# Kernel tuning notes

Hardware: AMD Instinct MI355X
Metric: run time of the kernel (lower is better)

## Reference

```python
import jax, jax.numpy as jnp
import numpy as np

NUM_HEADS = 12
EPS = 1e-6


def setup_inputs() -> dict:
    key = jax.random.key(0)
    k1, k2, k3, k4, k5 = jax.random.split(key, 5)
    B, N, C = 8, 4096, 768
    scale = 1.0 / np.sqrt(C)
    return {
        "x": jax.random.normal(k1, (B, N, C), dtype=jnp.float32),
        "W_qkv": jax.random.normal(k2, (C, 3 * C), dtype=jnp.float32) * scale,
        "b_qkv": jax.random.normal(k3, (3 * C,), dtype=jnp.float32) * 0.02,
        "W_proj": jax.random.normal(k4, (C, C), dtype=jnp.float32) * scale,
        "b_proj": jax.random.normal(k5, (C,), dtype=jnp.float32) * 0.02,
    }


def reference(x, W_qkv, b_qkv, W_proj, b_proj):
    B, N, C = x.shape
    H = NUM_HEADS
    D = C // H
    # qkv projection -> (3, B, H, N, D)
    qkv = (x @ W_qkv + b_qkv).reshape(B, N, 3, H, D).transpose(2, 0, 3, 1, 4)
    q, k, v = qkv[0], qkv[1], qkv[2]
    q = jax.nn.sigmoid(q)
    k = jax.nn.sigmoid(k)
    ksum = k.sum(axis=2)  # [B,H,D]
    qsum = q.sum(axis=2)  # [B,H,D]
    # incoming/outgoing flow normalizers, [B,H,N]
    sink_incoming = 1.0 / (jnp.einsum('bhnd,bhd->bhn', q + EPS, ksum + EPS) + EPS)
    source_outgoing = 1.0 / (jnp.einsum('bhnd,bhd->bhn', k + EPS, qsum + EPS) + EPS)
    conserved_sink = jnp.einsum(
        'bhnd,bhd->bhn', q + EPS, (k * source_outgoing[..., None]).sum(axis=2) + EPS) + EPS
    conserved_source = jnp.einsum(
        'bhnd,bhd->bhn', k + EPS, (q * sink_incoming[..., None]).sum(axis=2) + EPS) + EPS
    conserved_source = jnp.clip(conserved_source, -1.0, 1.0)
    sink_allocation = jax.nn.sigmoid(conserved_sink * (float(N) / float(N)))
    source_competition = jax.nn.softmax(conserved_source, axis=-1) * float(N)
    # linear attention: kv = k^T @ (v * competition), [B,H,D,D]
    kv = jnp.einsum('bhnd,bhne->bhde', k, v * source_competition[..., None])
    x_update = jnp.einsum('bhnd,bhde->bhne', q, kv)
    x_update = x_update * sink_incoming[..., None] * sink_allocation[..., None]
    out = x_update.transpose(0, 2, 1, 3).reshape(B, N, C)
    out = out @ W_proj + b_proj
    return jax.nn.sigmoid(2.0 * out)
```

## Files before the change

### kernel.cpp

```cpp
#include <hip/hip_runtime.h>
#include <stdint.h>

#define EPSF 1e-6f

typedef unsigned short u16;
typedef __attribute__((ext_vector_type(8))) short short8;
typedef __attribute__((ext_vector_type(4))) float f32x4;

__device__ __forceinline__ float us2f(u16 u) {
  union { float f; unsigned int i; } c; c.i = ((unsigned int)u) << 16; return c.f;
}
__device__ __forceinline__ u16 f2bfu(float f) {
  union { float f; unsigned int i; } c; c.f = f;
  unsigned int i = c.i;
  return (u16)((i + 0x7FFFu + ((i >> 16) & 1u)) >> 16);
}
__device__ __forceinline__ float sigm(float x) { return 1.f / (1.f + __expf(-x)); }

typedef __attribute__((address_space(3))) unsigned int lds_u32;
typedef const __attribute__((address_space(1))) unsigned int glb_u32;
__device__ __forceinline__ void gl_lds16(const u16* g, u16* l) {
  __builtin_amdgcn_global_load_lds((glb_u32*)g, (lds_u32*)l, 16, 0, 0);
}

__global__ void k_cvt_x(const float* __restrict__ in, u16* __restrict__ out) {
  const int i = blockIdx.x * 256 + threadIdx.x;
  float4 v = ((const float4*)in)[i];
  ushort4 o;
  o.x = f2bfu(v.x); o.y = f2bfu(v.y); o.z = f2bfu(v.z); o.w = f2bfu(v.w);
  ((ushort4*)out)[i] = o;
}

__global__ void k_transpose(const float* __restrict__ in, u16* __restrict__ out, int R, int C) {
  __shared__ float tile[32][33];
  const int tx = threadIdx.x & 31, ty = threadIdx.x >> 5;
  const int c0 = blockIdx.x << 5, r0 = blockIdx.y << 5;
  for (int i = ty; i < 32; i += 8) tile[i][tx] = in[(size_t)(r0 + i) * C + c0 + tx];
  __syncthreads();
  for (int i = ty; i < 32; i += 8) out[(size_t)(c0 + i) * R + r0 + tx] = f2bfu(tile[tx][i]);
}

template <int MODE>
__global__ __launch_bounds__(512, 2) void k_gemm(
    const u16* __restrict__ A, const u16* __restrict__ BT,
    const float* __restrict__ bias,
    u16* __restrict__ qkvo, float* __restrict__ qsum, float* __restrict__ ksum,
    float* __restrict__ outf)
{
  __shared__ __align__(16) u16 smem[65536];
  const int tid = threadIdx.x;
  const int lane = tid & 63;
  const int wid = tid >> 6;
  const int wm = wid >> 2, wn = wid & 3;
  const int nx = gridDim.x;
  int lid = blockIdx.y * nx + blockIdx.x;
  const int q8 = (nx * gridDim.y) >> 3;
  lid = (lid & 7) * q8 + (lid >> 3);
  const int m0 = (lid / nx) << 8;
  const int n0 = (lid % nx) << 8;

  const int rowS = tid >> 2;
  const int sub  = tid & 3;
  const int subx = sub ^ ((rowS >> 1) & 3);
  const u16* gA = A  + (size_t)(m0 + rowS) * 768 + (subx << 3);
  const u16* gB = BT + (size_t)(n0 + rowS) * 768 + (subx << 3);
  const int dstc = tid << 3;

  const int r16 = lane & 15;
  const int sgrp = lane >> 4;
  int offA[8], offB[4];
#pragma unroll
  for (int mi = 0; mi < 8; ++mi) {
    const int ra = (wm << 7) + (mi << 4) + r16;
    offA[mi] = ra * 32 + ((sgrp ^ ((ra >> 1) & 3)) << 3);
  }
#pragma unroll
  for (int nj = 0; nj < 4; ++nj) {
    const int rb = (wn << 6) + (nj << 4) + r16;
    offB[nj] = rb * 32 + ((sgrp ^ ((rb >> 1) & 3)) << 3);
  }

  f32x4 acc[8][4];
#pragma unroll
  for (int i = 0; i < 8; ++i)
#pragma unroll
    for (int j = 0; j < 4; ++j) acc[i][j] = (f32x4){0.f, 0.f, 0.f, 0.f};

#define STAGE(kh)                                                   \
  do {                                                              \
    const int khs = ((kh) > 23 ? 23 : (kh)) << 5;                   \
    const int so = ((kh) & 3) << 13;                                \
    gl_lds16(gA + khs,         &smem[so + dstc]);                   \
    gl_lds16(gA + 98304 + khs, &smem[so + dstc + 4096]);            \
    gl_lds16(gB + khs,         &smem[32768 + so + dstc]);           \
    gl_lds16(gB + 98304 + khs, &smem[32768 + so + dstc + 4096]);    \
  } while (0)

  STAGE(0); STAGE(1); STAGE(2);

  for (int kh = 0; kh < 24; ++kh) {
    asm volatile("s_waitcnt vmcnt(8)" ::: "memory");
    __builtin_amdgcn_s_barrier();
    __builtin_amdgcn_sched_barrier(0);
    STAGE(kh + 3);
    const u16* pa = &smem[(kh & 3) << 13];
    const u16* pb = pa + 32768;
    short8 bf[4];
#pragma unroll
    for (int nj = 0; nj < 4; ++nj) bf[nj] = *(const short8*)(pb + offB[nj]);
    __builtin_amdgcn_s_setprio(1);
#pragma unroll
    for (int mi = 0; mi < 8; ++mi) {
      const short8 av = *(const short8*)(pa + offA[mi]);
#pragma unroll
      for (int nj = 0; nj < 4; ++nj)
        acc[mi][nj] = __builtin_amdgcn_mfma_f32_16x16x32_bf16(av, bf[nj], acc[mi][nj], 0, 0, 0);
    }
    __builtin_amdgcn_s_setprio(0);
  }
#undef STAGE
  asm volatile("s_waitcnt vmcnt(0)" ::: "memory");

  if (MODE == 0) {
    const int colc = n0 + (wn << 6);
    const bool sg = (colc < 1536);
    float jsum[4] = {0.f, 0.f, 0.f, 0.f};
#pragma unroll
    for (int mi = 0; mi < 8; ++mi) {
      const int rowb = m0 + (wm << 7) + (mi << 4) + ((lane >> 4) << 2);
#pragma unroll
      for (int nj = 0; nj < 4; ++nj) {
        const int col = colc + (nj << 4) + r16;
        const float bcol = bias[col];
        if (sg) {
#pragma unroll
          for (int rg = 0; rg < 4; ++rg) {
            const float val = sigm(acc[mi][nj][rg] + bcol);
            jsum[nj] += val;
            qkvo[(size_t)(rowb + rg) * 2304 + col] = f2bfu(val);
          }
        } else {
#pragma unroll
          for (int rg = 0; rg < 4; ++rg)
            qkvo[(size_t)(rowb + rg) * 2304 + col] = f2bfu(acc[mi][nj][rg] + bcol);
        }
      }
    }
    if (sg) {
#pragma unroll
      for (int nj = 0; nj < 4; ++nj) {
        jsum[nj] += __shfl_xor(jsum[nj], 16, 64);
        jsum[nj] += __shfl_xor(jsum[nj], 32, 64);
      }
      if (lane < 16) {
        const int b12 = (m0 >> 12) * 12;
        float* sdst = (colc >= 768) ? ksum : qsum;
        const int cb = (colc >= 768) ? colc - 768 : colc;
#pragma unroll
        for (int nj = 0; nj < 4; ++nj)
          atomicAdd(&sdst[(b12 << 6) + cb + (nj << 4) + r16], jsum[nj]);
      }
    }
  } else {
#pragma unroll
    for (int mi = 0; mi < 8; ++mi) {
      const int rowb = m0 + (wm << 7) + (mi << 4) + ((lane >> 4) << 2);
#pragma unroll
      for (int nj = 0; nj < 4; ++nj) {
        const int col = n0 + (wn << 6) + (nj << 4) + r16;
        const float bcol = bias[col];
#pragma unroll
        for (int rg = 0; rg < 4; ++rg)
          outf[(size_t)(rowb + rg) * 768 + col] = sigm(2.f * (acc[mi][nj][rg] + bcol));
      }
    }
  }
}

__global__ __launch_bounds__(256) void k_flow1(
    const u16* __restrict__ qkv,
    const float* __restrict__ qsum, const float* __restrict__ ksum,
    float* __restrict__ si_out, float* __restrict__ qsi, float* __restrict__ kso)
{
  const int bh = blockIdx.x >> 3, sp = blockIdx.x & 7;
  const int tid = threadIdx.x;
  const int grp = tid >> 3;
  const int d0 = (tid & 7) << 3;
  const u16* base = qkv + (size_t)(bh / 12) * 4096 * 2304 + (bh % 12) * 64;

  float ke[8], qe[8];
#pragma unroll
  for (int u = 0; u < 8; ++u) {
    ke[u] = ksum[(bh << 6) + d0 + u] + EPSF;
    qe[u] = qsum[(bh << 6) + d0 + u] + EPSF;
  }
  float Sk = 0.f, Sq = 0.f;
#pragma unroll
  for (int u = 0; u < 8; ++u) { Sk += ke[u]; Sq += qe[u]; }
#pragma unroll
  for (int m = 1; m < 8; m <<= 1) { Sk += __shfl_xor(Sk, m, 64); Sq += __shfl_xor(Sq, m, 64); }
  const float cK = EPSF * Sk + EPSF;
  const float cQ = EPSF * Sq + EPSF;

  float aq[8], ak[8];
#pragma unroll
  for (int u = 0; u < 8; ++u) { aq[u] = 0.f; ak[u] = 0.f; }

  const int nbase = sp << 9;
  for (int it = 0; it < 16; ++it) {
    const int n = nbase + (it << 5) + grp;
    const u16* rp = base + (size_t)n * 2304 + d0;
    short8 q8 = *(const short8*)(rp);
    short8 k8 = *(const short8*)(rp + 768);
    float dq = 0.f, dk = 0.f;
#pragma unroll
    for (int u = 0; u < 8; ++u) {
      dq += us2f((u16)q8[u]) * ke[u];
      dk += us2f((u16)k8[u]) * qe[u];
    }
#pragma unroll
    for (int m = 1; m < 8; m <<= 1) { dq += __shfl_xor(dq, m, 64); dk += __shfl_xor(dk, m, 64); }
    const float si = 1.f / (dq + cK);
    const float so = 1.f / (dk + cQ);
    if ((tid & 7) == 0) si_out[(bh << 12) + n] = si;
#pragma unroll
    for (int u = 0; u < 8; ++u) {
      aq[u] += us2f((u16)q8[u]) * si;
      ak[u] += us2f((u16)k8[u]) * so;
    }
  }
  __shared__ float redq[32][68];
  __shared__ float redk[32][68];
#pragma unroll
  for (int u = 0; u < 8; ++u) { redq[grp][d0 + u] = aq[u]; redk[grp][d0 + u] = ak[u]; }
  __syncthreads();
  if (tid < 128) {
    const int which = tid >> 6, d = tid & 63;
    float s = 0.f;
    if (which == 0) {
#pragma unroll
      for (int g = 0; g < 32; ++g) s += redq[g][d];
      atomicAdd(&qsi[(bh << 6) + d], s);
    } else {
#pragma unroll
      for (int g = 0; g < 32; ++g) s += redk[g][d];
      atomicAdd(&kso[(bh << 6) + d], s);
    }
  }
}

__global__ __launch_bounds__(256) void k_fkv(
    const u16* __restrict__ qkv,
    const float* __restrict__ qsi, const float* __restrict__ kso,
    const float* __restrict__ si_in,
    float* __restrict__ mo, float* __restrict__ sumexp, float* __restrict__ kvm)
{
  __shared__ __align__(16) u16 smem[2 * 64 * 136];
  u16* kT = smem;
  u16* vT = smem + 64 * 136;
  const int tid = threadIdx.x;
  const int bh = blockIdx.x >> 3, sp = blockIdx.x & 7;
  const int lane = tid & 63, wid = tid >> 6;
  const int r16 = lane & 15, g = lane >> 4;
  const u16* base = qkv + (size_t)(bh / 12) * 4096 * 2304 + (bh % 12) * 64;
  const float* sib = si_in + ((size_t)bh << 12);
  float* mob = mo + ((size_t)bh << 12);

  const int d0 = (tid & 7) << 3;
  float qie[8], soe[8];
#pragma unroll
  for (int u = 0; u < 8; ++u) {
    qie[u] = qsi[(bh << 6) + d0 + u] + EPSF;
    soe[u] = kso[(bh << 6) + d0 + u] + EPSF;
  }
  float Sq = qsi[(bh << 6) + lane] + EPSF;
  float Sk = kso[(bh << 6) + lane] + EPSF;
#pragma unroll
  for (int m = 1; m < 64; m <<= 1) { Sq += __shfl_xor(Sq, m, 64); Sk += __shfl_xor(Sk, m, 64); }
  const float cR = EPSF * Sq + EPSF;
  const float cS = EPSF * Sk + EPSF;

  f32x4 acc[4][4];
#pragma unroll
  for (int i = 0; i < 4; ++i)
#pragma unroll
    for (int j = 0; j < 4; ++j) acc[i][j] = (f32x4){0.f, 0.f, 0.f, 0.f};

  const int nf = (wid << 5) + (g << 3);
  float esum = 0.f;

  for (int st = 0; st < 4; ++st) {
    const int nst = (sp << 9) + (st << 7);
#pragma unroll
    for (int i = 0; i < 4; ++i) {
      const int c = tid + (i << 8);
      const int nl = c >> 3;
      const int ng = nst + nl;
      const u16* rp = base + (size_t)ng * 2304 + d0;
      short8 q8 = *(const short8*)(rp);
      short8 k8 = *(const short8*)(rp + 768);
      short8 v8 = *(const short8*)(rp + 1536);
      float pcs = 0.f, pcr = 0.f;
#pragma unroll
      for (int u = 0; u < 8; ++u) {
        pcs += us2f((u16)q8[u]) * soe[u];
        pcr += us2f((u16)k8[u]) * qie[u];
      }
#pragma unroll
      for (int m = 1; m < 8; m <<= 1) { pcs += __shfl_xor(pcs, m, 64); pcr += __shfl_xor(pcr, m, 64); }
      float cr = pcr + cR;
      cr = fminf(1.f, fmaxf(-1.f, cr));
      const float ev = __expf(cr);
      const int col = nl ^ (d0 & 56);
#pragma unroll
      for (int u = 0; u < 8; ++u) {
        kT[(d0 + u) * 136 + col] = f2bfu(us2f((u16)k8[u]) * ev);
        vT[(d0 + u) * 136 + col] = (u16)(unsigned short)v8[u];
      }
      if ((tid & 7) == 0) {
        mob[ng] = sib[ng] * sigm(pcs + cS);
        esum += ev;
      }
    }
    __syncthreads();

    short8 af[4], bf[4];
#pragma unroll
    for (int mi = 0; mi < 4; ++mi) {
      const int row = (mi << 4) + r16;
      af[mi] = *(const short8*)&kT[row * 136 + (nf ^ (row & 56))];
    }
#pragma unroll
    for (int nj = 0; nj < 4; ++nj) {
      const int row = (nj << 4) + r16;
      bf[nj] = *(const short8*)&vT[row * 136 + (nf ^ (row & 56))];
    }
#pragma unroll
    for (int mi = 0; mi < 4; ++mi)
#pragma unroll
      for (int nj = 0; nj < 4; ++nj)
        acc[mi][nj] = __builtin_amdgcn_mfma_f32_16x16x32_bf16(af[mi], bf[nj], acc[mi][nj], 0, 0, 0);
    __syncthreads();
  }

  float* red = (float*)smem;
  float* kvb = kvm + ((size_t)bh << 12);
#pragma unroll
  for (int half = 0; half < 2; ++half) {
#pragma unroll
    for (int m2 = 0; m2 < 2; ++m2) {
      const int mi = (half << 1) + m2;
#pragma unroll
      for (int nj = 0; nj < 4; ++nj)
#pragma unroll
        for (int rg = 0; rg < 4; ++rg)
          red[(wid << 11) + (((m2 << 4) + (g << 2) + rg) << 6) + (nj << 4) + r16] = acc[mi][nj][rg];
    }
    __syncthreads();
    const int base2 = tid << 3;
#pragma unroll
    for (int u2 = 0; u2 < 2; ++u2) {
      const int o = base2 + (u2 << 2);
      float4 s0 = *(const float4*)&red[o];
      float4 s1 = *(const float4*)&red[2048 + o];
      float4 s2 = *(const float4*)&red[4096 + o];
      float4 s3 = *(const float4*)&red[6144 + o];
      s0.x += s1.x + s2.x + s3.x;
      s0.y += s1.y + s2.y + s3.y;
      s0.z += s1.z + s2.z + s3.z;
      s0.w += s1.w + s2.w + s3.w;
      const int gi = (half << 11) + o;
      atomicAdd(&kvb[gi + 0], s0.x);
      atomicAdd(&kvb[gi + 1], s0.y);
      atomicAdd(&kvb[gi + 2], s0.z);
      atomicAdd(&kvb[gi + 3], s0.w);
    }
    __syncthreads();
  }

  esum += __shfl_xor(esum, 8, 64);
  esum += __shfl_xor(esum, 16, 64);
  esum += __shfl_xor(esum, 32, 64);
  if (lane == 0) atomicAdd(&sumexp[bh], esum);
}

__global__ __launch_bounds__(256) void k_xup(
    const u16* __restrict__ qkv, const float* __restrict__ kvm,
    const float* __restrict__ m_arr, const float* __restrict__ sumexp,
    u16* __restrict__ attn)
{
  const int bh = blockIdx.y;
  const int n0 = blockIdx.x << 7;
  const int b = bh / 12, h = bh % 12;
  __shared__ __align__(16) u16 qs[128 * 72];
  __shared__ __align__(16) u16 kvs[64 * 72];
  const int tid = threadIdx.x, lane = tid & 63, wid = tid >> 6;
  const u16* qg = qkv + (size_t)b * 4096 * 2304 + (size_t)n0 * 2304 + h * 64;
#pragma unroll
  for (int i = 0; i < 4; ++i) {
    const int c = tid + (i << 8);
    const int nl = c >> 3, d0 = (c & 7) << 3;
    *(short8*)&qs[nl * 72 + d0] = *(const short8*)(qg + (size_t)nl * 2304 + d0);
  }
  const float* kvg = kvm + ((size_t)bh << 12);
#pragma unroll
  for (int i = 0; i < 4; ++i) {
    const int idx = (tid << 2) + (i << 10);
    const int d = idx >> 6, e0 = idx & 63;
    float4 vv = *(const float4*)(kvg + idx);
    kvs[(e0 + 0) * 72 + d] = f2bfu(vv.x);
    kvs[(e0 + 1) * 72 + d] = f2bfu(vv.y);
    kvs[(e0 + 2) * 72 + d] = f2bfu(vv.z);
    kvs[(e0 + 3) * 72 + d] = f2bfu(vv.w);
  }
  __syncthreads();
  const float scale = 4096.f / sumexp[bh];
  const int r16 = lane & 15, kg8 = (lane >> 4) << 3;
  f32x4 acc[2][4];
#pragma unroll
  for (int i = 0; i < 2; ++i)
#pragma unroll
    for (int j = 0; j < 4; ++j) acc[i][j] = (f32x4){0.f, 0.f, 0.f, 0.f};
#pragma unroll
  for (int kk = 0; kk < 2; ++kk) {
    short8 af[2], bfv[4];
#pragma unroll
    for (int mi = 0; mi < 2; ++mi)
      af[mi] = *(const short8*)&qs[((wid << 5) + (mi << 4) + r16) * 72 + (kk << 5) + kg8];
#pragma unroll
    for (int nj = 0; nj < 4; ++nj)
      bfv[nj] = *(const short8*)&kvs[((nj << 4) + r16) * 72 + (kk << 5) + kg8];
#pragma unroll
    for (int mi = 0; mi < 2; ++mi)
#pragma unroll
      for (int nj = 0; nj < 4; ++nj)
        acc[mi][nj] = __builtin_amdgcn_mfma_f32_16x16x32_bf16(af[mi], bfv[nj], acc[mi][nj], 0, 0, 0);
  }
#pragma unroll
  for (int mi = 0; mi < 2; ++mi) {
#pragma unroll
    for (int rg = 0; rg < 4; ++rg) {
      const int n = n0 + (wid << 5) + (mi << 4) + ((lane >> 4) << 2) + rg;
      const float mult = m_arr[((size_t)bh << 12) + n] * scale;
#pragma unroll
      for (int nj = 0; nj < 4; ++nj) {
        const int e = (nj << 4) + r16;
        attn[((size_t)(b * 4096 + n)) * 768 + (h << 6) + e] = f2bfu(acc[mi][nj][rg] * mult);
      }
    }
  }
}

extern "C" void kernel_launch(void* const* d_in, const int* in_sizes, int n_in,
                              void* d_out, int out_size, void* d_ws, size_t ws_size,
                              hipStream_t stream)
{
  (void)in_sizes; (void)n_in; (void)out_size; (void)ws_size;
  const float* x     = (const float*)d_in[0];
  const float* Wqkv  = (const float*)d_in[1];
  const float* bqkv  = (const float*)d_in[2];
  const float* Wproj = (const float*)d_in[3];
  const float* bproj = (const float*)d_in[4];
  float* out = (float*)d_out;

  char* ws = (char*)d_ws;
  size_t off = 0;
  auto alloc = [&](size_t bytes) -> char* {
    char* p = ws + off;
    off += (bytes + 255) & ~(size_t)255;
    return p;
  };
  u16* qkv  = (u16*)alloc(150994944);
  u16* xbf  = (u16*)alloc(50331648);
  u16* WqT  = (u16*)alloc(3538944);
  u16* WpT  = (u16*)alloc(1179648);
  float* si = (float*)alloc(1572864);
  float* mb = (float*)alloc(1572864);
  char* zbase = ws + off;
  float* qsum   = (float*)alloc(24576);
  float* ksum   = (float*)alloc(24576);
  float* qsi    = (float*)alloc(24576);
  float* kso    = (float*)alloc(24576);
  float* sumexp = (float*)alloc(512);
  float* kvm    = (float*)alloc(1572864);
  const size_t zbytes = (size_t)((ws + off) - zbase);

  hipMemsetAsync(zbase, 0, zbytes, stream);
  k_cvt_x<<<24576, 256, 0, stream>>>(x, xbf);
  k_transpose<<<dim3(72, 24), 256, 0, stream>>>(Wqkv, WqT, 768, 2304);
  k_transpose<<<dim3(24, 24), 256, 0, stream>>>(Wproj, WpT, 768, 768);
  k_gemm<0><<<dim3(9, 128), 512, 0, stream>>>(xbf, WqT, bqkv, qkv, qsum, ksum, nullptr);
  k_flow1<<<768, 256, 0, stream>>>(qkv, qsum, ksum, si, qsi, kso);
  k_fkv<<<768, 256, 0, stream>>>(qkv, qsi, kso, si, mb, sumexp, kvm);
  k_xup<<<dim3(32, 96), 256, 0, stream>>>(qkv, kvm, mb, sumexp, xbf);
  k_gemm<1><<<dim3(3, 128), 512, 0, stream>>>(xbf, WpT, bproj, nullptr, nullptr, nullptr, out);
}
```

Baseline: 412.0 us.

## Restructure GEMM main loop into phased ping-pong schedule with 64-wide K tiles

The bf16 GEMM main loop is rewritten. The K step goes from 32 to 64, so there are 12 iterations instead of 24. A 4-stage ring buffer is replaced by double buffering, and each iteration is split into four barrier-separated MFMA phases. The global-to-LDS loads for the next tile are interleaved between those phases, and the LDS swizzle is changed to an 8-chunk XOR pattern. Launch bounds drop to one block per CU, so the compiler may use more registers. This trades occupancy and prefetch depth for tighter overlap of loads with MFMA work and fewer barriers per K element.

```diff
diff --git a/kernel.cpp b/kernel.cpp
--- a/kernel.cpp
+++ b/kernel.cpp
@@ -41,7 +41,7 @@
 }
 
 template <int MODE>
-__global__ __launch_bounds__(512, 2) void k_gemm(
+__global__ __launch_bounds__(512, 1) void k_gemm(
     const u16* __restrict__ A, const u16* __restrict__ BT,
     const float* __restrict__ bias,
     u16* __restrict__ qkvo, float* __restrict__ qsum, float* __restrict__ ksum,
@@ -59,26 +59,17 @@
   const int m0 = (lid / nx) << 8;
   const int n0 = (lid % nx) << 8;
 
-  const int rowS = tid >> 2;
-  const int sub  = tid & 3;
-  const int subx = sub ^ ((rowS >> 1) & 3);
-  const u16* gA = A  + (size_t)(m0 + rowS) * 768 + (subx << 3);
-  const u16* gB = BT + (size_t)(n0 + rowS) * 768 + (subx << 3);
-  const int dstc = tid << 3;
+  const int rowL0 = tid >> 3;
+  const int gc = (tid & 7) ^ (rowL0 & 7);
+  const u16* gA = A  + (size_t)(m0 + rowL0) * 768 + (gc << 3);
+  const u16* gB = BT + (size_t)(n0 + rowL0) * 768 + (gc << 3);
 
   const int r16 = lane & 15;
   const int sgrp = lane >> 4;
-  int offA[8], offB[4];
-#pragma unroll
-  for (int mi = 0; mi < 8; ++mi) {
-    const int ra = (wm << 7) + (mi << 4) + r16;
-    offA[mi] = ra * 32 + ((sgrp ^ ((ra >> 1) & 3)) << 3);
-  }
-#pragma unroll
-  for (int nj = 0; nj < 4; ++nj) {
-    const int rb = (wn << 6) + (nj << 4) + r16;
-    offB[nj] = rb * 32 + ((sgrp ^ ((rb >> 1) & 3)) << 3);
-  }
+  const int xk = r16 & 7;
+  const int coff0 = ((sgrp) ^ xk) << 3;
+  const int coff1 = ((4 + sgrp) ^ xk) << 3;
+  const int bbase = ((wn & 1) << 6) + r16;
 
   f32x4 acc[8][4];
 #pragma unroll
@@ -86,40 +77,93 @@
 #pragma unroll
     for (int j = 0; j < 4; ++j) acc[i][j] = (f32x4){0.f, 0.f, 0.f, 0.f};
 
-#define STAGE(kh)                                                   \
-  do {                                                              \
-    const int khs = ((kh) > 23 ? 23 : (kh)) << 5;                   \
-    const int so = ((kh) & 3) << 13;                                \
-    gl_lds16(gA + khs,         &smem[so + dstc]);                   \
-    gl_lds16(gA + 98304 + khs, &smem[so + dstc + 4096]);            \
-    gl_lds16(gB + khs,         &smem[32768 + so + dstc]);           \
-    gl_lds16(gB + 98304 + khs, &smem[32768 + so + dstc + 4096]);    \
+#define STAGEU(tt, y)                                                         \
+  do {                                                                        \
+    u16* dst = &smem[(((((tt) & 1) << 2) | (y)) << 13) + (tid << 3)];         \
+    const u16* s = (((y) < 2) ? gA + (size_t)(y) * 98304                      \
+                              : gB + (size_t)((y) - 2) * 98304) + (tt) * 64;  \
+    gl_lds16(s, dst);                                                         \
+    gl_lds16(s + 49152, dst + 4096);                                          \
   } while (0)
 
-  STAGE(0); STAGE(1); STAGE(2);
-
-  for (int kh = 0; kh < 24; ++kh) {
-    asm volatile("s_waitcnt vmcnt(8)" ::: "memory");
+#define RDA(mi, co) (*(const short8*)(pa + ((((mi) << 4) + r16) << 6) + (co)))
+#define RDB(nj, co) (*(const short8*)(pb + ((bbase + ((nj) << 4)) << 6) + (co)))
+
+#define MFMA16(P, A00, A01, A10, A11)                                                               \
+  do {                                                                                              \
+    acc[2*(P)  ][0] = __builtin_amdgcn_mfma_f32_16x16x32_bf16(A00, bf[0][0], acc[2*(P)  ][0],0,0,0);\
+    acc[2*(P)  ][1] = __builtin_amdgcn_mfma_f32_16x16x32_bf16(A00, bf[1][0], acc[2*(P)  ][1],0,0,0);\
+    acc[2*(P)  ][2] = __builtin_amdgcn_mfma_f32_16x16x32_bf16(A00, bf[2][0], acc[2*(P)  ][2],0,0,0);\
+    acc[2*(P)  ][3] = __builtin_amdgcn_mfma_f32_16x16x32_bf16(A00, bf[3][0], acc[2*(P)  ][3],0,0,0);\
+    acc[2*(P)+1][0] = __builtin_amdgcn_mfma_f32_16x16x32_bf16(A10, bf[0][0], acc[2*(P)+1][0],0,0,0);\
+    acc[2*(P)+1][1] = __builtin_amdgcn_mfma_f32_16x16x32_bf16(A10, bf[1][0], acc[2*(P)+1][1],0,0,0);\
+    acc[2*(P)+1][2] = __builtin_amdgcn_mfma_f32_16x16x32_bf16(A10, bf[2][0], acc[2*(P)+1][2],0,0,0);\
+    acc[2*(P)+1][3] = __builtin_amdgcn_mfma_f32_16x16x32_bf16(A10, bf[3][0], acc[2*(P)+1][3],0,0,0);\
+    acc[2*(P)  ][0] = __builtin_amdgcn_mfma_f32_16x16x32_bf16(A01, bf[0][1], acc[2*(P)  ][0],0,0,0);\
+    acc[2*(P)  ][1] = __builtin_amdgcn_mfma_f32_16x16x32_bf16(A01, bf[1][1], acc[2*(P)  ][1],0,0,0);\
+    acc[2*(P)  ][2] = __builtin_amdgcn_mfma_f32_16x16x32_bf16(A01, bf[2][1], acc[2*(P)  ][2],0,0,0);\
+    acc[2*(P)  ][3] = __builtin_amdgcn_mfma_f32_16x16x32_bf16(A01, bf[3][1], acc[2*(P)  ][3],0,0,0);\
+    acc[2*(P)+1][0] = __builtin_amdgcn_mfma_f32_16x16x32_bf16(A11, bf[0][1], acc[2*(P)+1][0],0,0,0);\
+    acc[2*(P)+1][1] = __builtin_amdgcn_mfma_f32_16x16x32_bf16(A11, bf[1][1], acc[2*(P)+1][1],0,0,0);\
+    acc[2*(P)+1][2] = __builtin_amdgcn_mfma_f32_16x16x32_bf16(A11, bf[2][1], acc[2*(P)+1][2],0,0,0);\
+    acc[2*(P)+1][3] = __builtin_amdgcn_mfma_f32_16x16x32_bf16(A11, bf[3][1], acc[2*(P)+1][3],0,0,0);\
+  } while (0)
+
+#define PH_SYNC_PRE()                                          \
+    __builtin_amdgcn_s_barrier();                              \
+    asm volatile("s_waitcnt lgkmcnt(0)" ::: "memory");         \
+    __builtin_amdgcn_sched_barrier(0);                         \
+    __builtin_amdgcn_s_setprio(1)
+
+#define PH_SYNC_POST()                                         \
+    __builtin_amdgcn_s_setprio(0);                             \
+    __builtin_amdgcn_sched_barrier(0);                         \
+    __builtin_amdgcn_s_barrier()
+
+  STAGEU(0, 0); STAGEU(0, 1); STAGEU(0, 2); STAGEU(0, 3);
+  asm volatile("s_waitcnt vmcnt(0)" ::: "memory");
+  __builtin_amdgcn_s_barrier();
+
+  for (int t = 0; t < 12; ++t) {
+    const u16* pa = &smem[((((t & 1) << 2) | wm) << 13)];
+    const u16* pb = &smem[((((t & 1) << 2) | (2 + (wn >> 1))) << 13)];
+    short8 bf[4][2];
+    bf[0][0] = RDB(0, coff0); bf[0][1] = RDB(0, coff1);
+    bf[1][0] = RDB(1, coff0); bf[1][1] = RDB(1, coff1);
+    bf[2][0] = RDB(2, coff0); bf[2][1] = RDB(2, coff1);
+    bf[3][0] = RDB(3, coff0); bf[3][1] = RDB(3, coff1);
+    short8 a00 = RDA(0, coff0), a01 = RDA(0, coff1);
+    short8 a10 = RDA(1, coff0), a11 = RDA(1, coff1);
+    if (t < 11) { STAGEU(t + 1, 0); STAGEU(t + 1, 1); }
+    PH_SYNC_PRE();
+    MFMA16(0, a00, a01, a10, a11);
+    PH_SYNC_POST();
+    a00 = RDA(2, coff0); a01 = RDA(2, coff1);
+    a10 = RDA(3, coff0); a11 = RDA(3, coff1);
+    if (t < 11) { STAGEU(t + 1, 2); STAGEU(t + 1, 3); }
+    PH_SYNC_PRE();
+    MFMA16(1, a00, a01, a10, a11);
+    PH_SYNC_POST();
+    a00 = RDA(4, coff0); a01 = RDA(4, coff1);
+    a10 = RDA(5, coff0); a11 = RDA(5, coff1);
+    PH_SYNC_PRE();
+    MFMA16(2, a00, a01, a10, a11);
+    PH_SYNC_POST();
+    a00 = RDA(6, coff0); a01 = RDA(6, coff1);
+    a10 = RDA(7, coff0); a11 = RDA(7, coff1);
+    PH_SYNC_PRE();
+    MFMA16(3, a00, a01, a10, a11);
+    __builtin_amdgcn_s_setprio(0);
+    __builtin_amdgcn_sched_barrier(0);
+    asm volatile("s_waitcnt vmcnt(0)" ::: "memory");
     __builtin_amdgcn_s_barrier();
-    __builtin_amdgcn_sched_barrier(0);
-    STAGE(kh + 3);
-    const u16* pa = &smem[(kh & 3) << 13];
-    const u16* pb = pa + 32768;
-    short8 bf[4];
-#pragma unroll
-    for (int nj = 0; nj < 4; ++nj) bf[nj] = *(const short8*)(pb + offB[nj]);
-    __builtin_amdgcn_s_setprio(1);
-#pragma unroll
-    for (int mi = 0; mi < 8; ++mi) {
-      const short8 av = *(const short8*)(pa + offA[mi]);
-#pragma unroll
-      for (int nj = 0; nj < 4; ++nj)
-        acc[mi][nj] = __builtin_amdgcn_mfma_f32_16x16x32_bf16(av, bf[nj], acc[mi][nj], 0, 0, 0);
-    }
-    __builtin_amdgcn_s_setprio(0);
-  }
-#undef STAGE
-  asm volatile("s_waitcnt vmcnt(0)" ::: "memory");
+  }
+#undef PH_SYNC_PRE
+#undef PH_SYNC_POST
+#undef MFMA16
+#undef RDA
+#undef RDB
+#undef STAGEU
 
   if (MODE == 0) {
     const int colc = n0 + (wn << 6);
```

After: 411.7 us. No clear change (-0.1%).
